# Kernel optimization log

Measured on AMD Instinct MI355X. Metric: run time of the kernel, lower is better.

The kernel has to match this reference:

```python
import jax, jax.numpy as jnp
import numpy as np


def setup_inputs() -> dict:
    key = jax.random.key(0)
    ks = jax.random.split(key, 8)
    N, E = 100000, 3200000
    IN, H, OUT = 256, 128, 64
    x = jax.random.normal(ks[0], (N, IN), dtype=jnp.float32)
    src = jax.random.randint(ks[1], (E,), 0, N, dtype=jnp.int64)
    dst = jax.random.randint(ks[2], (E,), 0, N, dtype=jnp.int64)
    # Glorot-ish scaled weights
    W1_self = jax.random.normal(ks[3], (IN, H), dtype=jnp.float32) / np.sqrt(IN)
    W1_neigh = jax.random.normal(ks[4], (IN, H), dtype=jnp.float32) / np.sqrt(IN)
    b1 = jnp.zeros((H,), dtype=jnp.float32)
    W2_self = jax.random.normal(ks[5], (H, OUT), dtype=jnp.float32) / np.sqrt(H)
    W2_neigh = jax.random.normal(ks[6], (H, OUT), dtype=jnp.float32) / np.sqrt(H)
    b2 = jnp.zeros((OUT,), dtype=jnp.float32)
    return {"x": x, "src": src, "dst": dst,
            "W1_self": W1_self, "W1_neigh": W1_neigh, "b1": b1,
            "W2_self": W2_self, "W2_neigh": W2_neigh, "b2": b2}


def _sage_mean(h, src, dst, W_self, W_neigh, b, deg_inv):
    # mean aggregation over in-neighbors (edges src -> dst)
    N = h.shape[0]
    agg = jax.ops.segment_sum(h[src], dst, num_segments=N)  # [N, F]
    h_neigh = agg * deg_inv[:, None]
    return h @ W_self + h_neigh @ W_neigh + b


def reference(x, src, dst, W1_self, W1_neigh, b1, W2_self, W2_neigh, b2):
    N = x.shape[0]
    deg = jax.ops.segment_sum(jnp.ones_like(dst, dtype=x.dtype), dst, num_segments=N)
    deg_inv = 1.0 / jnp.maximum(deg, 1.0)  # DGL clamps in-degree to >= 1
    h = _sage_mean(x, src, dst, W1_self, W1_neigh, b1, deg_inv)
    h = jax.nn.relu(h)
    h = _sage_mean(h, src, dst, W2_self, W2_neigh, b2, deg_inv)
    return h
```

## Files before the change

kernel.cpp:

```cpp
#include <hip/hip_runtime.h>
#include <hip/hip_bf16.h>


typedef unsigned int uint32;
typedef __attribute__((ext_vector_type(8))) short short8;
typedef __attribute__((ext_vector_type(4))) float f32x4;

#define NBMAX 1024
#define EPB   8192

#if defined(__has_builtin)
#if __has_builtin(__builtin_amdgcn_cvt_pk_f32_fp8) && __has_builtin(__builtin_amdgcn_cvt_pk_fp8_f32)
#define FP8_HW 1
#endif
#endif
#ifndef FP8_HW
#define FP8_HW 0
#endif

__device__ __forceinline__ unsigned short f2bf(float f) {
    unsigned u = __float_as_uint(f);
    u += 0x7fffu + ((u >> 16) & 1u);
    return (unsigned short)(u >> 16);
}
__device__ __forceinline__ uint32 pack2bf(float lo, float hi) {
    return (uint32)f2bf(lo) | ((uint32)f2bf(hi) << 16);
}
__device__ __forceinline__ float bf_lo(uint32 v) { return __uint_as_float(v << 16); }
__device__ __forceinline__ float bf_hi(uint32 v) { return __uint_as_float(v & 0xFFFF0000u); }

__device__ __forceinline__ unsigned char enc8(float v) {
#if FP8_HW
    return (unsigned char)(__builtin_amdgcn_cvt_pk_fp8_f32(v, v, 0, false) & 0xFF);
#else
    float g = v * 0x1p-120f;
    uint32 b = __float_as_uint(g);
    uint32 s = (b >> 24) & 0x80u;
    b &= 0x7fffffffu;
    b += 0x7ffffu + ((b >> 20) & 1u);
    int t = (int)(b >> 20) - 960;
    t = t < 0 ? 0 : (t > 126 ? 126 : t);
    return (unsigned char)(s | (uint32)t);
#endif
}
#if !FP8_HW
__device__ __forceinline__ float dec1(uint32 b) {
    uint32 bits = ((b & 0x80u) << 24) | ((b & 0x7fu) << 20);
    return __uint_as_float(bits) * 0x1p+120f;
}
#endif
__device__ __forceinline__ void dec_u32(uint32 u, float& f0, float& f1, float& f2, float& f3) {
#if FP8_HW
    auto lo = __builtin_amdgcn_cvt_pk_f32_fp8(u, false);
    auto hi = __builtin_amdgcn_cvt_pk_f32_fp8(u, true);
    f0 = lo[0]; f1 = lo[1]; f2 = hi[0]; f3 = hi[1];
#else
    f0 = dec1(u & 0xffu); f1 = dec1((u >> 8) & 0xffu);
    f2 = dec1((u >> 16) & 0xffu); f3 = dec1(u >> 24);
#endif
}

__global__ __launch_bounds__(256) void k_bucket_count(const int* __restrict__ dst, int E,
                                                      int* __restrict__ bcnt) {
    __shared__ int hist[NBMAX];
    for (int i = threadIdx.x; i < NBMAX; i += 256) hist[i] = 0;
    __syncthreads();
    int base = blockIdx.x * EPB;
    #pragma unroll 4
    for (int i = 0; i < EPB / 256; ++i) {
        int e = base + i * 256 + threadIdx.x;
        if (e < E) atomicAdd(&hist[dst[e] >> 7], 1);
    }
    __syncthreads();
    for (int i = threadIdx.x; i < NBMAX; i += 256) {
        int h = hist[i];
        if (h) atomicAdd(&bcnt[i], h);
    }
}

__global__ __launch_bounds__(1024) void k_bucket_scan(const int* __restrict__ bcnt, int NB,
                                                      int* __restrict__ boffs, int* __restrict__ gfill,
                                                      int E) {
    __shared__ int sd[1024];
    int tid = threadIdx.x;
    int v = (tid < NB) ? bcnt[tid] : 0;
    sd[tid] = v;
    __syncthreads();
    for (int off = 1; off < 1024; off <<= 1) {
        int t = (tid >= off) ? sd[tid - off] : 0;
        __syncthreads();
        sd[tid] += t;
        __syncthreads();
    }
    int excl = sd[tid] - v;
    if (tid < NB) { boffs[tid] = excl; gfill[tid] = excl; }
    if (tid == 0) boffs[NB] = E;
}

__global__ __launch_bounds__(256) void k_bucket_scatter(const int* __restrict__ src,
                                                        const int* __restrict__ dst, int E,
                                                        int* __restrict__ gfill,
                                                        uint32* __restrict__ pairs) {
    __shared__ int hist[NBMAX];
    __shared__ int basea[NBMAX];
    for (int i = threadIdx.x; i < NBMAX; i += 256) hist[i] = 0;
    __syncthreads();
    int base = blockIdx.x * EPB;
    #pragma unroll 4
    for (int i = 0; i < EPB / 256; ++i) {
        int e = base + i * 256 + threadIdx.x;
        if (e < E) atomicAdd(&hist[dst[e] >> 7], 1);
    }
    __syncthreads();
    for (int i = threadIdx.x; i < NBMAX; i += 256) {
        int h = hist[i];
        basea[i] = h ? atomicAdd(&gfill[i], h) : 0;
        hist[i] = 0;
    }
    __syncthreads();
    #pragma unroll 4
    for (int i = 0; i < EPB / 256; ++i) {
        int e = base + i * 256 + threadIdx.x;
        if (e < E) {
            int d = dst[e];
            int b = d >> 7;
            int pos = basea[b] + atomicAdd(&hist[b], 1);
            pairs[pos] = ((uint32)src[e] << 7) | (uint32)(d & 127);
        }
    }
}

__global__ __launch_bounds__(256) void k_bucket_sort(const uint32* __restrict__ pairs,
                                                     const int* __restrict__ boffs,
                                                     int N, int E,
                                                     int* __restrict__ row_start,
                                                     float* __restrict__ deg_inv,
                                                     int* __restrict__ src_sorted) {
    __shared__ int cnt[128];
    __shared__ int sc[128];
    __shared__ int fill[128];
    int b = blockIdx.x, tid = threadIdx.x;
    int s0 = boffs[b], s1 = boffs[b + 1];
    if (tid < 128) cnt[tid] = 0;
    __syncthreads();
    for (int e = s0 + tid; e < s1; e += 256)
        atomicAdd(&cnt[pairs[e] & 127], 1);
    __syncthreads();
    if (tid < 128) sc[tid] = cnt[tid];
    __syncthreads();
    for (int off = 1; off < 128; off <<= 1) {
        int v = 0;
        if (tid < 128 && tid >= off) v = sc[tid - off];
        __syncthreads();
        if (tid < 128) sc[tid] += v;
        __syncthreads();
    }
    if (tid < 128) {
        int excl = sc[tid] - cnt[tid];
        int node = b * 128 + tid;
        if (node < N) {
            row_start[node] = s0 + excl;
            int d = cnt[tid];
            deg_inv[node] = 1.0f / (float)(d > 1 ? d : 1);
        }
        fill[tid] = s0 + excl;
    }
    if (b == 0 && tid == 0) row_start[N] = E;
    __syncthreads();
    for (int e = s0 + tid; e < s1; e += 256) {
        uint32 p = pairs[e];
        int pos = atomicAdd(&fill[p & 127], 1);
        src_sorted[pos] = (int)(p >> 7);
    }
}

__global__ __launch_bounds__(256) void k_wt(const float* __restrict__ Ws, const float* __restrict__ Wn,
                                            int K, int logK, int halfC, unsigned short* __restrict__ Wt) {
    int t = blockIdx.x * blockDim.x + threadIdx.x;
    int total = 2 * halfC * K;
    if (t >= total) return;
    int c = t >> logK, k = t & (K - 1);
    float v = (c < halfC) ? Ws[(size_t)k * halfC + c] : Wn[(size_t)k * halfC + (c - halfC)];
    Wt[t] = f2bf(v);
}

template<int K, int NF, bool AF32, bool YSPLIT>
__global__ __launch_bounds__(256) void gemm_rs(const void* __restrict__ Aptr, int Arows, int nstrip,
                                               const unsigned short* __restrict__ Wt,
                                               unsigned short* __restrict__ S16,
                                               unsigned char* __restrict__ N8) {
    constexpr int KS = K / 32;
    __shared__ unsigned short Bs[NF * KS * 512];
    const int tid = threadIdx.x;
    const int wave = tid >> 6, lane = tid & 63;
    const int l15 = lane & 15, l4 = lane >> 4;

    const int ycol = YSPLIT ? blockIdx.y * 64 : 0;
    const unsigned short* Wtblk = Wt + (size_t)ycol * K;
    const bool out8 = YSPLIT && (blockIdx.y >= 2);
    const int ybase = YSPLIT ? (blockIdx.y & 1) * 64 : 0;

    for (int i = tid; i < NF * KS * 64; i += 256) {
        int f = i >> 6, l = i & 63;
        int s = f / NF, n = f - s * NF;
        int col = n * 16 + (l & 15);
        int k = s * 32 + (l >> 4) * 8;
        uint4 v = *reinterpret_cast<const uint4*>(&Wtblk[(size_t)col * K + k]);
        *reinterpret_cast<uint4*>(&Bs[(size_t)i * 8]) = v;
    }
    __syncthreads();

    const unsigned short* Bl = Bs + (size_t)lane * 8;
    const int stride = gridDim.x;
    int g = blockIdx.x;
    if (g >= nstrip) return;

    float4 a[AF32 ? 2 * KS : 1];
    uint4  ub[AF32 ? 1 : KS];

    auto loadA = [&](int gg) {
        int arow = gg * 64 + wave * 16 + l15;
        if constexpr (AF32) {
            int r = arow < Arows ? arow : Arows - 1;
            const float* Ar = (const float*)Aptr + (size_t)r * K + l4 * 8;
            #pragma unroll
            for (int s = 0; s < KS; ++s) {
                a[2 * s]     = *reinterpret_cast<const float4*>(Ar + s * 32);
                a[2 * s + 1] = *reinterpret_cast<const float4*>(Ar + s * 32 + 4);
            }
        } else {
            const unsigned short* Ar = (const unsigned short*)Aptr + (size_t)arow * K + l4 * 8;
            #pragma unroll
            for (int s = 0; s < KS; ++s)
                ub[s] = *reinterpret_cast<const uint4*>(Ar + s * 32);
        }
    };

    loadA(g);
    while (true) {
        short8 af[KS];
        if constexpr (AF32) {
            #pragma unroll
            for (int s = 0; s < KS; ++s) {
                union { uint32 u[4]; short8 v; } cv;
                cv.u[0] = pack2bf(a[2*s].x,   a[2*s].y);
                cv.u[1] = pack2bf(a[2*s].z,   a[2*s].w);
                cv.u[2] = pack2bf(a[2*s+1].x, a[2*s+1].y);
                cv.u[3] = pack2bf(a[2*s+1].z, a[2*s+1].w);
                af[s] = cv.v;
            }
        } else {
            #pragma unroll
            for (int s = 0; s < KS; ++s) {
                union { uint4 q; short8 v; } cv;
                cv.q = ub[s];
                af[s] = cv.v;
            }
        }
        int gn = g + stride;
        if (gn < nstrip) loadA(gn);

        f32x4 acc[NF] = {};
        #pragma unroll
        for (int s = 0; s < KS; ++s) {
            #pragma unroll
            for (int n = 0; n < NF; ++n) {
                short8 bf = *reinterpret_cast<const short8*>(Bl + (size_t)(s * NF + n) * 512);
                acc[n] = __builtin_amdgcn_mfma_f32_16x16x32_bf16(af[s], bf, acc[n], 0, 0, 0);
            }
        }
        const int rbase = g * 64 + wave * 16;
        #pragma unroll
        for (int n = 0; n < NF; ++n) {
            #pragma unroll
            for (int r = 0; r < 4; ++r) {
                int rw = rbase + l4 * 4 + r;
                if constexpr (YSPLIT) {
                    int col = ybase + n * 16 + l15;
                    if (out8) N8[(size_t)rw * 128 + col] = enc8(acc[n][r]);
                    else      S16[(size_t)rw * 128 + col] = f2bf(acc[n][r]);
                } else {
                    if (n < 4) S16[(size_t)rw * 64 + n * 16 + l15] = f2bf(acc[n][r]);
                    else       N8[(size_t)rw * 64 + (n - 4) * 16 + l15] = enc8(acc[n][r]);
                }
            }
        }
        if (gn >= nstrip) break;
        g = gn;
    }
}

__global__ __launch_bounds__(256) void k_agg1(const uint2* __restrict__ t1n, const uint4* __restrict__ t1s,
                                              const int* __restrict__ rs, const int* __restrict__ ss,
                                              const float* __restrict__ dinv, const float* __restrict__ b1,
                                              uint4* __restrict__ h, int N) {
    int wid  = (blockIdx.x * blockDim.x + threadIdx.x) >> 6;
    int lane = threadIdx.x & 63;
    if (wid >= N) return;
    int e0 = rs[wid], e1 = rs[wid + 1];
    const int q = lane >> 4, c = lane & 15;
    float a0 = 0, a1 = 0, a2 = 0, a3 = 0, a4 = 0, a5 = 0, a6 = 0, a7 = 0;
    float f0, f1, f2, f3;
    int e = e0;
    for (; e + 16 <= e1; e += 16) {
        int s0 = ss[e + q];
        int s1 = ss[e + 4 + q];
        int s2 = ss[e + 8 + q];
        int s3 = ss[e + 12 + q];
        uint2 v0 = t1n[(size_t)s0 * 16 + c];
        uint2 v1 = t1n[(size_t)s1 * 16 + c];
        uint2 v2 = t1n[(size_t)s2 * 16 + c];
        uint2 v3 = t1n[(size_t)s3 * 16 + c];
        dec_u32(v0.x, f0, f1, f2, f3); a0 += f0; a1 += f1; a2 += f2; a3 += f3;
        dec_u32(v0.y, f0, f1, f2, f3); a4 += f0; a5 += f1; a6 += f2; a7 += f3;
        dec_u32(v1.x, f0, f1, f2, f3); a0 += f0; a1 += f1; a2 += f2; a3 += f3;
        dec_u32(v1.y, f0, f1, f2, f3); a4 += f0; a5 += f1; a6 += f2; a7 += f3;
        dec_u32(v2.x, f0, f1, f2, f3); a0 += f0; a1 += f1; a2 += f2; a3 += f3;
        dec_u32(v2.y, f0, f1, f2, f3); a4 += f0; a5 += f1; a6 += f2; a7 += f3;
        dec_u32(v3.x, f0, f1, f2, f3); a0 += f0; a1 += f1; a2 += f2; a3 += f3;
        dec_u32(v3.y, f0, f1, f2, f3); a4 += f0; a5 += f1; a6 += f2; a7 += f3;
    }
    for (; e < e1; e += 4) {
        if (e + q < e1) {
            int s = ss[e + q];
            uint2 v = t1n[(size_t)s * 16 + c];
            dec_u32(v.x, f0, f1, f2, f3); a0 += f0; a1 += f1; a2 += f2; a3 += f3;
            dec_u32(v.y, f0, f1, f2, f3); a4 += f0; a5 += f1; a6 += f2; a7 += f3;
        }
    }
    a0 += __shfl_xor(a0, 16); a1 += __shfl_xor(a1, 16); a2 += __shfl_xor(a2, 16); a3 += __shfl_xor(a3, 16);
    a4 += __shfl_xor(a4, 16); a5 += __shfl_xor(a5, 16); a6 += __shfl_xor(a6, 16); a7 += __shfl_xor(a7, 16);
    a0 += __shfl_xor(a0, 32); a1 += __shfl_xor(a1, 32); a2 += __shfl_xor(a2, 32); a3 += __shfl_xor(a3, 32);
    a4 += __shfl_xor(a4, 32); a5 += __shfl_xor(a5, 32); a6 += __shfl_xor(a6, 32); a7 += __shfl_xor(a7, 32);
    if (lane < 16) {
        float di = dinv[wid];
        uint4 sv = t1s[(size_t)wid * 16 + c];
        float4 bA = *reinterpret_cast<const float4*>(&b1[c * 8]);
        float4 bB = *reinterpret_cast<const float4*>(&b1[c * 8 + 4]);
        float h0 = fmaxf(fmaf(a0, di, bf_lo(sv.x)) + bA.x, 0.f);
        float h1 = fmaxf(fmaf(a1, di, bf_hi(sv.x)) + bA.y, 0.f);
        float h2 = fmaxf(fmaf(a2, di, bf_lo(sv.y)) + bA.z, 0.f);
        float h3 = fmaxf(fmaf(a3, di, bf_hi(sv.y)) + bA.w, 0.f);
        float h4 = fmaxf(fmaf(a4, di, bf_lo(sv.z)) + bB.x, 0.f);
        float h5 = fmaxf(fmaf(a5, di, bf_hi(sv.z)) + bB.y, 0.f);
        float h6 = fmaxf(fmaf(a6, di, bf_lo(sv.w)) + bB.z, 0.f);
        float h7 = fmaxf(fmaf(a7, di, bf_hi(sv.w)) + bB.w, 0.f);
        uint4 o;
        o.x = pack2bf(h0, h1); o.y = pack2bf(h2, h3);
        o.z = pack2bf(h4, h5); o.w = pack2bf(h6, h7);
        h[(size_t)wid * 16 + c] = o;
    }
}

__global__ __launch_bounds__(256) void k_agg2(const uint2* __restrict__ t2n, const uint4* __restrict__ t2s,
                                              const int* __restrict__ rs, const int* __restrict__ ss,
                                              const float* __restrict__ dinv, const float* __restrict__ b2,
                                              float* __restrict__ out, int N) {
    int wid  = (blockIdx.x * blockDim.x + threadIdx.x) >> 6;
    int lane = threadIdx.x & 63;
    if (wid >= N) return;
    int e0 = rs[wid], e1 = rs[wid + 1];
    const int o8 = lane >> 3, c = lane & 7;
    float a0 = 0, a1 = 0, a2 = 0, a3 = 0, a4 = 0, a5 = 0, a6 = 0, a7 = 0;
    float f0, f1, f2, f3;
    int e = e0;
    for (; e + 32 <= e1; e += 32) {
        int s0 = ss[e + o8];
        int s1 = ss[e + 8 + o8];
        int s2 = ss[e + 16 + o8];
        int s3 = ss[e + 24 + o8];
        uint2 v0 = t2n[(size_t)s0 * 8 + c];
        uint2 v1 = t2n[(size_t)s1 * 8 + c];
        uint2 v2 = t2n[(size_t)s2 * 8 + c];
        uint2 v3 = t2n[(size_t)s3 * 8 + c];
        dec_u32(v0.x, f0, f1, f2, f3); a0 += f0; a1 += f1; a2 += f2; a3 += f3;
        dec_u32(v0.y, f0, f1, f2, f3); a4 += f0; a5 += f1; a6 += f2; a7 += f3;
        dec_u32(v1.x, f0, f1, f2, f3); a0 += f0; a1 += f1; a2 += f2; a3 += f3;
        dec_u32(v1.y, f0, f1, f2, f3); a4 += f0; a5 += f1; a6 += f2; a7 += f3;
        dec_u32(v2.x, f0, f1, f2, f3); a0 += f0; a1 += f1; a2 += f2; a3 += f3;
        dec_u32(v2.y, f0, f1, f2, f3); a4 += f0; a5 += f1; a6 += f2; a7 += f3;
        dec_u32(v3.x, f0, f1, f2, f3); a0 += f0; a1 += f1; a2 += f2; a3 += f3;
        dec_u32(v3.y, f0, f1, f2, f3); a4 += f0; a5 += f1; a6 += f2; a7 += f3;
    }
    for (; e < e1; e += 8) {
        if (e + o8 < e1) {
            int s = ss[e + o8];
            uint2 v = t2n[(size_t)s * 8 + c];
            dec_u32(v.x, f0, f1, f2, f3); a0 += f0; a1 += f1; a2 += f2; a3 += f3;
            dec_u32(v.y, f0, f1, f2, f3); a4 += f0; a5 += f1; a6 += f2; a7 += f3;
        }
    }
    a0 += __shfl_xor(a0, 8);  a1 += __shfl_xor(a1, 8);  a2 += __shfl_xor(a2, 8);  a3 += __shfl_xor(a3, 8);
    a4 += __shfl_xor(a4, 8);  a5 += __shfl_xor(a5, 8);  a6 += __shfl_xor(a6, 8);  a7 += __shfl_xor(a7, 8);
    a0 += __shfl_xor(a0, 16); a1 += __shfl_xor(a1, 16); a2 += __shfl_xor(a2, 16); a3 += __shfl_xor(a3, 16);
    a4 += __shfl_xor(a4, 16); a5 += __shfl_xor(a5, 16); a6 += __shfl_xor(a6, 16); a7 += __shfl_xor(a7, 16);
    a0 += __shfl_xor(a0, 32); a1 += __shfl_xor(a1, 32); a2 += __shfl_xor(a2, 32); a3 += __shfl_xor(a3, 32);
    a4 += __shfl_xor(a4, 32); a5 += __shfl_xor(a5, 32); a6 += __shfl_xor(a6, 32); a7 += __shfl_xor(a7, 32);
    if (lane < 8) {
        float di = dinv[wid];
        uint4 sv = t2s[(size_t)wid * 8 + c];
        float4 bA = *reinterpret_cast<const float4*>(&b2[c * 8]);
        float4 bB = *reinterpret_cast<const float4*>(&b2[c * 8 + 4]);
        float4 oA, oB;
        oA.x = fmaf(a0, di, bf_lo(sv.x)) + bA.x;
        oA.y = fmaf(a1, di, bf_hi(sv.x)) + bA.y;
        oA.z = fmaf(a2, di, bf_lo(sv.y)) + bA.z;
        oA.w = fmaf(a3, di, bf_hi(sv.y)) + bA.w;
        oB.x = fmaf(a4, di, bf_lo(sv.z)) + bB.x;
        oB.y = fmaf(a5, di, bf_hi(sv.z)) + bB.y;
        oB.z = fmaf(a6, di, bf_lo(sv.w)) + bB.z;
        oB.w = fmaf(a7, di, bf_hi(sv.w)) + bB.w;
        *reinterpret_cast<float4*>(&out[(size_t)wid * 64 + c * 8]) = oA;
        *reinterpret_cast<float4*>(&out[(size_t)wid * 64 + c * 8 + 4]) = oB;
    }
}

extern "C" void kernel_launch(void* const* d_in, const int* in_sizes, int n_in,
                              void* d_out, int out_size, void* d_ws, size_t ws_size,
                              hipStream_t stream) {
    const float* x   = (const float*)d_in[0];
    const int*   src = (const int*)d_in[1];
    const int*   dst = (const int*)d_in[2];
    const float* W1s = (const float*)d_in[3];
    const float* W1n = (const float*)d_in[4];
    const float* b1  = (const float*)d_in[5];
    const float* W2s = (const float*)d_in[6];
    const float* W2n = (const float*)d_in[7];
    const float* b2  = (const float*)d_in[8];
    float* out = (float*)d_out;

    const int IN = 256, H = 128, OUT = 64;
    const int N  = in_sizes[0] / IN;
    const int E  = in_sizes[1];
    const int Mpad = (N + 127) & ~127;
    const int NB = (N + 127) >> 7;

    char* ws = (char*)d_ws;
    size_t off = 0;
    auto alloc = [&](size_t bytes) -> char* {
        char* p = ws + off;
        off = (off + bytes + 255) & ~(size_t)255;
        return p;
    };
    int*   row_start  = (int*)  alloc((size_t)(N + 1) * 4);
    float* deg_inv    = (float*)alloc((size_t)N * 4);
    int*   bcnt       = (int*)  alloc((size_t)NBMAX * 4);
    int*   boffs      = (int*)  alloc((size_t)(NBMAX + 1) * 4);
    int*   gfill      = (int*)  alloc((size_t)NBMAX * 4);
    int*   src_sorted = (int*)  alloc((size_t)E * 4);
    uint32* pairs     = (uint32*)alloc((size_t)E * 4);
    unsigned short* Wt1 = (unsigned short*)alloc((size_t)(2 * H) * IN * 2);
    unsigned short* Wt2 = (unsigned short*)alloc((size_t)(2 * OUT) * H * 2);
    unsigned short* t1s = (unsigned short*)alloc((size_t)Mpad * H * 2);
    unsigned char*  t1n = (unsigned char*) alloc((size_t)Mpad * H);
    unsigned short* hbf = (unsigned short*)alloc((size_t)Mpad * H * 2);

    hipMemsetAsync(bcnt, 0, (size_t)NBMAX * 4, stream);
    int nblk = (E + EPB - 1) / EPB;
    k_bucket_count  <<<nblk, 256, 0, stream>>>(dst, E, bcnt);
    k_bucket_scan   <<<1, 1024, 0, stream>>>(bcnt, NB, boffs, gfill, E);
    k_bucket_scatter<<<nblk, 256, 0, stream>>>(src, dst, E, gfill, pairs);
    k_bucket_sort   <<<NB, 256, 0, stream>>>(pairs, boffs, N, E, row_start, deg_inv, src_sorted);

    k_wt<<<(2 * H * IN + 255) / 256, 256, 0, stream>>>(W1s, W1n, IN, 8, H, Wt1);
    k_wt<<<(2 * OUT * H + 255) / 256, 256, 0, stream>>>(W2s, W2n, H, 7, OUT, Wt2);

    int nstrip1 = (N + 63) / 64;
    gemm_rs<256, 4, true, true><<<dim3(512, 4), 256, 0, stream>>>(x, N, nstrip1, Wt1, t1s, t1n);
    k_agg1<<<(N + 3) / 4, 256, 0, stream>>>((const uint2*)t1n, (const uint4*)t1s,
                                            row_start, src_sorted, deg_inv, b1, (uint4*)hbf, N);
    int nstrip2 = Mpad / 64;
    gemm_rs<128, 8, false, false><<<dim3(512, 1), 256, 0, stream>>>(hbf, Mpad, nstrip2, Wt2, t1s, t1n);
    k_agg2<<<(N + 3) / 4, 256, 0, stream>>>((const uint2*)t1n, (const uint4*)t1s,
                                            row_start, src_sorted, deg_inv, b2, out, N);
}
```

Measured before the change: 348.7 us.

## Pre-cast x to bf16, widen GEMM blocks to 512 threads with double-buffered A loads

Adds a separate kernel that converts x to padded bf16 once, so the first GEMM reads half as many bytes and the y-grid split drops from 4 to 2. Each GEMM block now has 8 waves covering 128 rows with NF=8 columns, and A tiles are double-buffered in two register sets. The aim is to cut redundant fp32 reads of x, which were repeated across y blocks, and to overlap loads with MFMA work. The cost is an extra pass that writes and rereads a bf16 copy of x, plus higher register pressure from the doubled A buffers.

Result: faster. 322.5 us (-7.5%).

```diff
diff --git a/kernel.cpp b/kernel.cpp
--- a/kernel.cpp
+++ b/kernel.cpp
@@ -174,6 +174,20 @@
     }
 }
 
+__global__ __launch_bounds__(256) void k_cast_x(const float* __restrict__ x, uint32* __restrict__ xb,
+                                                long n8, long total8) {
+    long t = (long)blockIdx.x * blockDim.x + threadIdx.x;
+    if (t >= total8) return;
+    uint4 o = make_uint4(0u, 0u, 0u, 0u);
+    if (t < n8) {
+        const float4* p = reinterpret_cast<const float4*>(x) + t * 2;
+        float4 a = p[0], b = p[1];
+        o.x = pack2bf(a.x, a.y); o.y = pack2bf(a.z, a.w);
+        o.z = pack2bf(b.x, b.y); o.w = pack2bf(b.z, b.w);
+    }
+    reinterpret_cast<uint4*>(xb)[t] = o;
+}
+
 __global__ __launch_bounds__(256) void k_wt(const float* __restrict__ Ws, const float* __restrict__ Wn,
                                             int K, int logK, int halfC, unsigned short* __restrict__ Wt) {
     int t = blockIdx.x * blockDim.x + threadIdx.x;
@@ -184,8 +198,8 @@
     Wt[t] = f2bf(v);
 }
 
-template<int K, int NF, bool AF32, bool YSPLIT>
-__global__ __launch_bounds__(256) void gemm_rs(const void* __restrict__ Aptr, int Arows, int nstrip,
+template<int K, int NF, bool YSPLIT>
+__global__ __launch_bounds__(512) void gemm_rs(const unsigned short* __restrict__ A, int nstrip,
                                                const unsigned short* __restrict__ Wt,
                                                unsigned short* __restrict__ S16,
                                                unsigned char* __restrict__ N8) {
@@ -195,12 +209,10 @@
     const int wave = tid >> 6, lane = tid & 63;
     const int l15 = lane & 15, l4 = lane >> 4;
 
-    const int ycol = YSPLIT ? blockIdx.y * 64 : 0;
-    const unsigned short* Wtblk = Wt + (size_t)ycol * K;
-    const bool out8 = YSPLIT && (blockIdx.y >= 2);
-    const int ybase = YSPLIT ? (blockIdx.y & 1) * 64 : 0;
-
-    for (int i = tid; i < NF * KS * 64; i += 256) {
+    const unsigned short* Wtblk = Wt + (YSPLIT ? (size_t)blockIdx.y * 128 * K : 0);
+    const bool out8 = YSPLIT && (blockIdx.y == 1);
+
+    for (int i = tid; i < NF * KS * 64; i += 512) {
         int f = i >> 6, l = i & 63;
         int s = f / NF, n = f - s * NF;
         int col = n * 16 + (l & 15);
@@ -215,68 +227,37 @@
     int g = blockIdx.x;
     if (g >= nstrip) return;
 
-    float4 a[AF32 ? 2 * KS : 1];
-    uint4  ub[AF32 ? 1 : KS];
-
-    auto loadA = [&](int gg) {
-        int arow = gg * 64 + wave * 16 + l15;
-        if constexpr (AF32) {
-            int r = arow < Arows ? arow : Arows - 1;
-            const float* Ar = (const float*)Aptr + (size_t)r * K + l4 * 8;
-            #pragma unroll
-            for (int s = 0; s < KS; ++s) {
-                a[2 * s]     = *reinterpret_cast<const float4*>(Ar + s * 32);
-                a[2 * s + 1] = *reinterpret_cast<const float4*>(Ar + s * 32 + 4);
-            }
-        } else {
-            const unsigned short* Ar = (const unsigned short*)Aptr + (size_t)arow * K + l4 * 8;
-            #pragma unroll
-            for (int s = 0; s < KS; ++s)
-                ub[s] = *reinterpret_cast<const uint4*>(Ar + s * 32);
-        }
+    uint4 uA[KS], uB[KS];
+
+    auto loadA = [&](int gg, uint4* u) {
+        int arow = gg * 128 + wave * 16 + l15;
+        const unsigned short* Ar = A + (size_t)arow * K + l4 * 8;
+        #pragma unroll
+        for (int s = 0; s < KS; ++s)
+            u[s] = *reinterpret_cast<const uint4*>(Ar + s * 32);
     };
 
-    loadA(g);
-    while (true) {
-        short8 af[KS];
-        if constexpr (AF32) {
-            #pragma unroll
-            for (int s = 0; s < KS; ++s) {
-                union { uint32 u[4]; short8 v; } cv;
-                cv.u[0] = pack2bf(a[2*s].x,   a[2*s].y);
-                cv.u[1] = pack2bf(a[2*s].z,   a[2*s].w);
-                cv.u[2] = pack2bf(a[2*s+1].x, a[2*s+1].y);
-                cv.u[3] = pack2bf(a[2*s+1].z, a[2*s+1].w);
-                af[s] = cv.v;
-            }
-        } else {
-            #pragma unroll
-            for (int s = 0; s < KS; ++s) {
-                union { uint4 q; short8 v; } cv;
-                cv.q = ub[s];
-                af[s] = cv.v;
-            }
-        }
-        int gn = g + stride;
-        if (gn < nstrip) loadA(gn);
-
+    auto compute = [&](int gc, uint4* u) {
         f32x4 acc[NF] = {};
         #pragma unroll
         for (int s = 0; s < KS; ++s) {
+            union { uint4 q; short8 v; } cv;
+            cv.q = u[s];
+            short8 af = cv.v;
             #pragma unroll
             for (int n = 0; n < NF; ++n) {
                 short8 bf = *reinterpret_cast<const short8*>(Bl + (size_t)(s * NF + n) * 512);
-                acc[n] = __builtin_amdgcn_mfma_f32_16x16x32_bf16(af[s], bf, acc[n], 0, 0, 0);
+                acc[n] = __builtin_amdgcn_mfma_f32_16x16x32_bf16(af, bf, acc[n], 0, 0, 0);
             }
         }
-        const int rbase = g * 64 + wave * 16;
+        const int rbase = gc * 128 + wave * 16;
         #pragma unroll
         for (int n = 0; n < NF; ++n) {
             #pragma unroll
             for (int r = 0; r < 4; ++r) {
                 int rw = rbase + l4 * 4 + r;
                 if constexpr (YSPLIT) {
-                    int col = ybase + n * 16 + l15;
+                    int col = n * 16 + l15;
                     if (out8) N8[(size_t)rw * 128 + col] = enc8(acc[n][r]);
                     else      S16[(size_t)rw * 128 + col] = f2bf(acc[n][r]);
                 } else {
@@ -285,6 +266,18 @@
                 }
             }
         }
+    };
+
+    loadA(g, uA);
+    while (true) {
+        int gn = g + stride;
+        if (gn < nstrip) loadA(gn, uB);
+        compute(g, uA);
+        if (gn >= nstrip) break;
+        g = gn;
+        gn = g + stride;
+        if (gn < nstrip) loadA(gn, uA);
+        compute(g, uB);
         if (gn >= nstrip) break;
         g = gn;
     }
@@ -449,6 +442,7 @@
     int*   gfill      = (int*)  alloc((size_t)NBMAX * 4);
     int*   src_sorted = (int*)  alloc((size_t)E * 4);
     uint32* pairs     = (uint32*)alloc((size_t)E * 4);
+    unsigned short* xb  = (unsigned short*)alloc((size_t)Mpad * IN * 2);
     unsigned short* Wt1 = (unsigned short*)alloc((size_t)(2 * H) * IN * 2);
     unsigned short* Wt2 = (unsigned short*)alloc((size_t)(2 * OUT) * H * 2);
     unsigned short* t1s = (unsigned short*)alloc((size_t)Mpad * H * 2);
@@ -462,15 +456,17 @@
     k_bucket_scatter<<<nblk, 256, 0, stream>>>(src, dst, E, gfill, pairs);
     k_bucket_sort   <<<NB, 256, 0, stream>>>(pairs, boffs, N, E, row_start, deg_inv, src_sorted);
 
+    long n8 = (long)N * IN / 8, total8 = (long)Mpad * IN / 8;
+    k_cast_x<<<(int)((total8 + 255) / 256), 256, 0, stream>>>(x, (uint32*)xb, n8, total8);
     k_wt<<<(2 * H * IN + 255) / 256, 256, 0, stream>>>(W1s, W1n, IN, 8, H, Wt1);
     k_wt<<<(2 * OUT * H + 255) / 256, 256, 0, stream>>>(W2s, W2n, H, 7, OUT, Wt2);
 
-    int nstrip1 = (N + 63) / 64;
-    gemm_rs<256, 4, true, true><<<dim3(512, 4), 256, 0, stream>>>(x, N, nstrip1, Wt1, t1s, t1n);
+    int nstrip1 = Mpad / 128;
+    gemm_rs<256, 8, true><<<dim3(256, 2), 512, 0, stream>>>(xb, nstrip1, Wt1, t1s, t1n);
     k_agg1<<<(N + 3) / 4, 256, 0, stream>>>((const uint2*)t1n, (const uint4*)t1s,
                                             row_start, src_sorted, deg_inv, b1, (uint4*)hbf, N);
-    int nstrip2 = Mpad / 64;
-    gemm_rs<128, 8, false, false><<<dim3(512, 1), 256, 0, stream>>>(hbf, Mpad, nstrip2, Wt2, t1s, t1n);
+    int nstrip2 = Mpad / 128;
+    gemm_rs<128, 8, false><<<dim3(256, 1), 512, 0, stream>>>(hbf, nstrip2, Wt2, t1s, t1n);
     k_agg2<<<(N + 3) / 4, 256, 0, stream>>>((const uint2*)t1n, (const uint4*)t1s,
                                             row_start, src_sorted, deg_inv, b2, out, N);
 }
```
